# Kernel tuning notes

Measured on AMD Instinct MI355X. Metric: run time of the kernel, lower is better.

Reference implementation:

```python
import jax, jax.numpy as jnp
import numpy as np

N_HEAD = 16

def setup_inputs() -> dict:
    key = jax.random.key(0)
    ks = jax.random.split(key, 4)
    B, S, D = 2, 2048, 2048
    return {
        "hidden_states": jax.random.normal(ks[0], (B, S, D), dtype=jnp.float32),
        "attention_mask": jnp.ones((B, S), dtype=jnp.float32),
        "W_attn": jax.random.normal(ks[1], (D, 3 * D), dtype=jnp.float32) * (D ** -0.5),
        "b_attn": jnp.zeros((3 * D,), dtype=jnp.float32),
        "W_proj": jax.random.normal(ks[2], (D, D), dtype=jnp.float32) * (D ** -0.5),
        "b_proj": jnp.zeros((D,), dtype=jnp.float32),
        "lambda_param": jnp.float32(0.8),
    }

def reference(hidden_states, attention_mask, W_attn, b_attn, W_proj, b_proj, lambda_param):
    B, S, D = hidden_states.shape
    H = N_HEAD
    hd = D // H          # full head dim (used by V and for the scale)
    qd = hd // 2         # q/k per-head dim after the dual chunk
    scale = hd ** -0.5

    qkv = hidden_states @ W_attn + b_attn            # [B,S,3D]
    q, k, v = jnp.split(qkv, 3, axis=-1)
    q1, q2 = jnp.split(q, 2, axis=-1)                # each [B,S,D/2]
    k1, k2 = jnp.split(k, 2, axis=-1)

    def heads(x, d):  # [B,S,H*d] -> [B,H,S,d]
        return x.reshape(B, S, H, d).transpose(0, 2, 1, 3)

    q1, q2 = heads(q1, qd), heads(q2, qd)
    k1, k2 = heads(k1, qd), heads(k2, qd)
    v = heads(v, hd)

    # additive mask: (1 - m) * -10000, broadcast over heads and query dim
    mask = (1.0 - attention_mask)[:, None, None, :] * -10000.0  # [B,1,1,S]

    s1 = jnp.einsum("bhqd,bhkd->bhqk", q1, k1) * scale + mask
    s2 = jnp.einsum("bhqd,bhkd->bhqk", q2, k2) * scale + mask
    w = jax.nn.softmax(s1, axis=-1) - lambda_param * jax.nn.softmax(s2, axis=-1)

    out = jnp.einsum("bhqk,bhkd->bhqd", w, v)        # [B,H,S,hd]
    out = out.transpose(0, 2, 1, 3).reshape(B, S, D)
    return out @ W_proj + b_proj
```

## Files before the change

### kernel.cpp

```cpp
#include <hip/hip_runtime.h>
#include <hip/hip_bf16.h>

typedef __attribute__((ext_vector_type(8))) short bf16x8;
typedef __attribute__((ext_vector_type(8))) unsigned short u16x8;
typedef __attribute__((ext_vector_type(4))) float f32x4;

__device__ __forceinline__ unsigned short f2bf(float f) {
  union { float f; unsigned int i; } v; v.f = f;
  unsigned int r = v.i + 0x7FFFu + ((v.i >> 16) & 1u);
  return (unsigned short)(r >> 16);
}
__device__ __forceinline__ unsigned int pack2bf_rn(float a, float b) {
  union { float f; unsigned int i; } x, y; x.f = a; y.f = b;
  return ((x.i + 0x8000u) >> 16) | ((y.i + 0x8000u) & 0xFFFF0000u);
}
__device__ __forceinline__ unsigned int cvtpk(float a, float b) {
  unsigned int r;
  asm("v_cvt_pk_bf16_f32 %0, %1, %2" : "=v"(r) : "v"(a), "v"(b));
  return r;
}
__device__ __forceinline__ float fexp2(float x) {
  float r;
  asm("v_exp_f32 %0, %1" : "=v"(r) : "v"(x));
  return r;
}
__device__ __forceinline__ void gll16(const unsigned short* g, unsigned short* l) {
  __builtin_amdgcn_global_load_lds(
      (const __attribute__((address_space(1))) unsigned int*)g,
      (__attribute__((address_space(3))) unsigned int*)l, 16, 0, 0);
}

__global__ void cvt_bf16_k(const float* __restrict__ in, unsigned short* __restrict__ out,
                           long n) {
  long i = ((long)blockIdx.x * 256 + threadIdx.x) * 8;
  if (i + 8 > n) return;
  float4 a = *(const float4*)(in + i);
  float4 b = *(const float4*)(in + i + 4);
  u16x8 o;
  o[0] = f2bf(a.x); o[1] = f2bf(a.y); o[2] = f2bf(a.z); o[3] = f2bf(a.w);
  o[4] = f2bf(b.x); o[5] = f2bf(b.y); o[6] = f2bf(b.z); o[7] = f2bf(b.w);
  *(u16x8*)(out + i) = o;
}

__global__ void cvt_transpose_k(const float* __restrict__ in, unsigned short* __restrict__ out,
                                long in_rs, long out_rs) {
  __shared__ unsigned short tile[32][33];
  int c0 = blockIdx.x * 32, r0 = blockIdx.y * 32;
  int tx = threadIdx.x & 31, ty = threadIdx.x >> 5;
#pragma unroll
  for (int i = 0; i < 32; i += 8)
    tile[ty + i][tx] = f2bf(in[(long)(r0 + ty + i) * in_rs + c0 + tx]);
  __syncthreads();
#pragma unroll
  for (int i = 0; i < 32; i += 8)
    out[(long)(c0 + ty + i) * out_rs + r0 + tx] = tile[tx][ty + i];
}

__global__ __launch_bounds__(256) void gemm_qkv(
    const unsigned short* __restrict__ A,
    const unsigned short* __restrict__ Bt,
    const float* __restrict__ bias,
    unsigned short* __restrict__ qQ,
    unsigned short* __restrict__ k1p, unsigned short* __restrict__ k2p,
    unsigned short* __restrict__ vp) {
  const int K = 2048;
  __shared__ unsigned short As[128 * 32];
  __shared__ unsigned short Bs[128 * 32];
  const int m0 = blockIdx.y * 128, n0 = blockIdx.x * 128;
  const int tid = threadIdx.x, lane = tid & 63, wave = tid >> 6;
  const int wm = (wave >> 1) * 64, wn = (wave & 1) * 64;
  const int quad = lane >> 4, l15 = lane & 15;
  const int ar = tid >> 2, ak = (tid & 3) * 8;

  f32x4 acc[4][4] = {};
  const unsigned short* Ap = A + (long)(m0 + ar) * K + ak;
  const unsigned short* Bp = Bt + (long)(n0 + ar) * K + ak;
  unsigned short* AsW = As + wave * 512;
  unsigned short* BsW = Bs + wave * 512;

  for (int kb = 0; kb < K; kb += 32) {
    __syncthreads();
    gll16(Ap + kb, AsW);
    gll16(Ap + (long)64 * K + kb, AsW + 2048);
    gll16(Bp + kb, BsW);
    gll16(Bp + (long)64 * K + kb, BsW + 2048);
    __syncthreads();
    bf16x8 af[4], bfr[4];
#pragma unroll
    for (int t = 0; t < 4; t++)
      af[t] = *(const bf16x8*)&As[(wm + t * 16 + l15) * 32 + quad * 8];
#pragma unroll
    for (int t = 0; t < 4; t++)
      bfr[t] = *(const bf16x8*)&Bs[(wn + t * 16 + l15) * 32 + quad * 8];
#pragma unroll
    for (int i = 0; i < 4; i++)
#pragma unroll
      for (int j = 0; j < 4; j++)
        acc[i][j] = __builtin_amdgcn_mfma_f32_16x16x32_bf16(af[i], bfr[j], acc[i][j], 0, 0, 0);
  }

  const int ncol = n0 + wn;
  if (ncol < 2048) {
#pragma unroll
    for (int j = 0; j < 4; j++) {
      int n = ncol + j * 16 + l15;
      float bv = bias[n];
#pragma unroll
      for (int i = 0; i < 4; i++) {
        int mr = m0 + wm + i * 16 + quad * 4;
#pragma unroll
        for (int r = 0; r < 4; r++)
          qQ[(long)(mr + r) * 2048 + n] = f2bf(acc[i][j][r] + bv);
      }
    }
  } else if (ncol < 4096) {
    unsigned short* kp = (ncol >= 3072) ? k2p : k1p;
#pragma unroll
    for (int j = 0; j < 4; j++) {
      int n = ncol + j * 16 + l15;
      float bv = bias[n];
      int kk = (n - 2048) & 1023;
      int h = kk >> 6, c = (kk >> 3) & 7, e = kk & 7;
#pragma unroll
      for (int i = 0; i < 4; i++) {
        int mr = m0 + wm + i * 16 + quad * 4;
        int b = mr >> 11, s = mr & 2047;
        long tb2 = ((long)(b * 16 + h) * 32 + (s >> 6)) * 4096 + e;
        int row0 = s & 63;
#pragma unroll
        for (int r = 0; r < 4; r++) {
          int row = row0 + r;
          kp[tb2 + row * 64 + ((c ^ (row & 7)) << 3)] = f2bf(acc[i][j][r] + bv);
        }
      }
    }
  } else {
#pragma unroll
    for (int j = 0; j < 4; j++) {
      int n = ncol + j * 16 + l15;
      float bv = bias[n];
      int vv = n - 4096;
      int h = vv >> 7, d = vv & 127;
#pragma unroll
      for (int i = 0; i < 4; i++) {
        int mr = m0 + wm + i * 16 + quad * 4;
        int b = mr >> 11, s = mr & 2047;
        int cc = (s & 63) >> 3;
        long dst = ((long)(b * 16 + h) * 32 + (s >> 6)) * 8192 + d * 64 +
                   ((cc ^ (d & 7)) << 3) + (quad & 1) * 4;
        uint2 st;
        st.x = pack2bf_rn(acc[i][j][0] + bv, acc[i][j][1] + bv);
        st.y = pack2bf_rn(acc[i][j][2] + bv, acc[i][j][3] + bv);
        *(uint2*)&vp[dst] = st;
      }
    }
  }
}

__global__ __launch_bounds__(256) void gemm_bt_f32(
    const unsigned short* __restrict__ A,
    const unsigned short* __restrict__ Bt,
    const float* __restrict__ bias,
    float* __restrict__ C, int K, int ldc) {
  __shared__ unsigned short As[128 * 32];
  __shared__ unsigned short Bs[128 * 32];
  const int m0 = blockIdx.y * 128, n0 = blockIdx.x * 128;
  const int tid = threadIdx.x, lane = tid & 63, wave = tid >> 6;
  const int wm = (wave >> 1) * 64, wn = (wave & 1) * 64;
  const int quad = lane >> 4, l15 = lane & 15;
  const int ar = tid >> 2, ak = (tid & 3) * 8;

  f32x4 acc[4][4] = {};
  const unsigned short* Ap = A + (long)(m0 + ar) * K + ak;
  const unsigned short* Bp = Bt + (long)(n0 + ar) * K + ak;
  unsigned short* AsW = As + wave * 512;
  unsigned short* BsW = Bs + wave * 512;

  for (int kb = 0; kb < K; kb += 32) {
    __syncthreads();
    gll16(Ap + kb, AsW);
    gll16(Ap + (long)64 * K + kb, AsW + 2048);
    gll16(Bp + kb, BsW);
    gll16(Bp + (long)64 * K + kb, BsW + 2048);
    __syncthreads();
    bf16x8 af[4], bfr[4];
#pragma unroll
    for (int t = 0; t < 4; t++)
      af[t] = *(const bf16x8*)&As[(wm + t * 16 + l15) * 32 + quad * 8];
#pragma unroll
    for (int t = 0; t < 4; t++)
      bfr[t] = *(const bf16x8*)&Bs[(wn + t * 16 + l15) * 32 + quad * 8];
#pragma unroll
    for (int i = 0; i < 4; i++)
#pragma unroll
      for (int j = 0; j < 4; j++)
        acc[i][j] = __builtin_amdgcn_mfma_f32_16x16x32_bf16(af[i], bfr[j], acc[i][j], 0, 0, 0);
  }
#pragma unroll
  for (int j = 0; j < 4; j++) {
    int n = n0 + wn + j * 16 + l15;
    float bv = bias[n];
#pragma unroll
    for (int i = 0; i < 4; i++) {
      int mr = m0 + wm + i * 16 + quad * 4;
#pragma unroll
      for (int r = 0; r < 4; r++)
        C[(long)(mr + r) * ldc + n] = acc[i][j][r] + bv;
    }
  }
}

__global__ __launch_bounds__(256, 2) void attn_k(
    const unsigned short* __restrict__ qQ,
    const unsigned short* __restrict__ k1p,
    const unsigned short* __restrict__ k2p,
    const unsigned short* __restrict__ vp,
    const float* __restrict__ mask,
    const float* __restrict__ lamp,
    unsigned short* __restrict__ out) {
  __shared__ unsigned short k1s[2 * 4096];
  __shared__ unsigned short k2s[2 * 4096];
  __shared__ unsigned short vts[2 * 8192];
  __shared__ unsigned short pls[4 * 2048];
  const int bid = blockIdx.x;
  const int wgid = (bid & 7) * 64 + (bid >> 3);
  const int bh = wgid >> 4;
  const int q0 = (wgid & 15) * 128;
  const int b = bh >> 4, h = bh & 15;
  const int tid = threadIdx.x, lane = tid & 63, wave = tid >> 6;
  const int quad = lane >> 4, l15 = lane & 15;
  const long rowq = (long)b * 2048 + q0;
  const int sw = l15 & 7;

  bf16x8 aq1[2][2], aq2[2][2];
#pragma unroll
  for (int qt = 0; qt < 2; qt++) {
    const unsigned short* qr =
        qQ + (rowq + wave * 32 + qt * 16 + l15) * 2048 + h * 64 + quad * 8;
    aq1[qt][0] = *(const bf16x8*)qr;
    aq1[qt][1] = *(const bf16x8*)(qr + 32);
    aq2[qt][0] = *(const bf16x8*)(qr + 1024);
    aq2[qt][1] = *(const bf16x8*)(qr + 1056);
  }
  f32x4 o1[2][8] = {}, o2[2][8] = {};
  f32x4 l1a[2] = {}, l2a[2] = {};
  bf16x8 ones;
#pragma unroll
  for (int e = 0; e < 8; e++) ones[e] = (short)0x3F80;
  const float SL = 0.08838834764831845f * 1.4426950408889634f;
  const float ML = 1.4426950408889634e4f;
  const long tb = (long)bh * 32;
  unsigned short* pw = pls + wave * 2048;

  {
    const unsigned short* k1t = k1p + tb * 4096 + tid * 8;
    const unsigned short* k2t = k2p + tb * 4096 + tid * 8;
    const unsigned short* vtt = vp + tb * 8192 + tid * 8;
    gll16(k1t, k1s + wave * 512);
    gll16(k1t + 2048, k1s + 2048 + wave * 512);
    gll16(k2t, k2s + wave * 512);
    gll16(k2t + 2048, k2s + 2048 + wave * 512);
#pragma unroll
    for (int rr = 0; rr < 4; rr++)
      gll16(vtt + rr * 2048, vts + rr * 2048 + wave * 512);
  }

  for (int t = 0; t < 32; t++) {
    const int cb = t & 1;
    __syncthreads();
    float4 mq[4];
#pragma unroll
    for (int nt = 0; nt < 4; nt++)
      mq[nt] = *(const float4*)(mask + (long)b * 2048 + t * 64 + nt * 16 + quad * 4);
    if (t < 31) {
      const unsigned short* k1t = k1p + (tb + t + 1) * 4096 + tid * 8;
      const unsigned short* k2t = k2p + (tb + t + 1) * 4096 + tid * 8;
      const unsigned short* vtt = vp + (tb + t + 1) * 8192 + tid * 8;
      unsigned short* d1 = k1s + (cb ^ 1) * 4096 + wave * 512;
      unsigned short* d2 = k2s + (cb ^ 1) * 4096 + wave * 512;
      unsigned short* dv = vts + (cb ^ 1) * 8192 + wave * 512;
      gll16(k1t, d1);
      gll16(k1t + 2048, d1 + 2048);
      gll16(k2t, d2);
      gll16(k2t + 2048, d2 + 2048);
#pragma unroll
      for (int rr = 0; rr < 4; rr++)
        gll16(vtt + rr * 2048, dv + rr * 2048);
    }

#pragma unroll
    for (int half = 0; half < 2; half++) {
      f32x4 s1[2][2] = {}, s2[2][2] = {};
#pragma unroll
      for (int np = 0; np < 2; np++) {
        const int row = cb * 4096 + (half * 32 + np * 16 + l15) * 64;
#pragma unroll
        for (int ks = 0; ks < 2; ks++) {
          const int p = ((ks * 4 + quad) ^ sw) * 8;
          bf16x8 kf1 = *(const bf16x8*)&k1s[row + p];
          bf16x8 kf2 = *(const bf16x8*)&k2s[row + p];
#pragma unroll
          for (int qt = 0; qt < 2; qt++) {
            s1[qt][np] = __builtin_amdgcn_mfma_f32_16x16x32_bf16(kf1, aq1[qt][ks], s1[qt][np], 0, 0, 0);
            s2[qt][np] = __builtin_amdgcn_mfma_f32_16x16x32_bf16(kf2, aq2[qt][ks], s2[qt][np], 0, 0, 0);
          }
        }
      }
      float ma[2][4];
#pragma unroll
      for (int np = 0; np < 2; np++)
#pragma unroll
        for (int r = 0; r < 4; r++)
          ma[np][r] = fmaf(((const float*)&mq[half * 2 + np])[r], ML, -ML);
#pragma unroll
      for (int qt = 0; qt < 2; qt++)
#pragma unroll
        for (int np = 0; np < 2; np++) {
          const int addr = l15 * 32 + (((np * 4 + quad) ^ sw) << 2);
          uint2 w1, w2;
          w1.x = cvtpk(fexp2(fmaf(s1[qt][np][0], SL, ma[np][0])),
                       fexp2(fmaf(s1[qt][np][1], SL, ma[np][1])));
          w1.y = cvtpk(fexp2(fmaf(s1[qt][np][2], SL, ma[np][2])),
                       fexp2(fmaf(s1[qt][np][3], SL, ma[np][3])));
          w2.x = cvtpk(fexp2(fmaf(s2[qt][np][0], SL, ma[np][0])),
                       fexp2(fmaf(s2[qt][np][1], SL, ma[np][1])));
          w2.y = cvtpk(fexp2(fmaf(s2[qt][np][2], SL, ma[np][2])),
                       fexp2(fmaf(s2[qt][np][3], SL, ma[np][3])));
          *(uint2*)&pw[(qt * 2 + 0) * 512 + addr] = w1;
          *(uint2*)&pw[(qt * 2 + 1) * 512 + addr] = w2;
        }
      asm volatile("s_waitcnt lgkmcnt(0)" ::: "memory");
      bf16x8 f1[2], f2[2];
      {
        const int ra = l15 * 32 + (((quad * 2 + 0) ^ sw) << 2);
        const int rb = l15 * 32 + (((quad * 2 + 1) ^ sw) << 2);
#pragma unroll
        for (int qt = 0; qt < 2; qt++) {
          union { bf16x8 v; uint2 u2[2]; } g1, g2;
          g1.u2[0] = *(const uint2*)&pw[(qt * 2 + 0) * 512 + ra];
          g1.u2[1] = *(const uint2*)&pw[(qt * 2 + 0) * 512 + rb];
          g2.u2[0] = *(const uint2*)&pw[(qt * 2 + 1) * 512 + ra];
          g2.u2[1] = *(const uint2*)&pw[(qt * 2 + 1) * 512 + rb];
          f1[qt] = g1.v; f2[qt] = g2.v;
        }
      }
#pragma unroll
      for (int qt = 0; qt < 2; qt++) {
        l1a[qt] = __builtin_amdgcn_mfma_f32_16x16x32_bf16(ones, f1[qt], l1a[qt], 0, 0, 0);
        l2a[qt] = __builtin_amdgcn_mfma_f32_16x16x32_bf16(ones, f2[qt], l2a[qt], 0, 0, 0);
      }
#pragma unroll
      for (int dn = 0; dn < 8; dn++) {
        const int pp = ((half * 4 + quad) ^ sw) * 8;
        bf16x8 vf = *(const bf16x8*)&vts[cb * 8192 + (dn * 16 + l15) * 64 + pp];
#pragma unroll
        for (int qt = 0; qt < 2; qt++) {
          o1[qt][dn] = __builtin_amdgcn_mfma_f32_16x16x32_bf16(vf, f1[qt], o1[qt][dn], 0, 0, 0);
          o2[qt][dn] = __builtin_amdgcn_mfma_f32_16x16x32_bf16(vf, f2[qt], o2[qt][dn], 0, 0, 0);
        }
      }
      asm volatile("s_waitcnt lgkmcnt(0)" ::: "memory");
    }
  }
  float lam = lamp[0];
#pragma unroll
  for (int qt = 0; qt < 2; qt++) {
    float i1 = 1.f / l1a[qt][0], i2 = lam / l2a[qt][0];
    unsigned short* orow =
        out + (rowq + wave * 32 + qt * 16 + l15) * 2048 + h * 128 + quad * 4;
#pragma unroll
    for (int dn = 0; dn < 8; dn++) {
      uint2 st;
      st.x = cvtpk(o1[qt][dn][0] * i1 - o2[qt][dn][0] * i2,
                   o1[qt][dn][1] * i1 - o2[qt][dn][1] * i2);
      st.y = cvtpk(o1[qt][dn][2] * i1 - o2[qt][dn][2] * i2,
                   o1[qt][dn][3] * i1 - o2[qt][dn][3] * i2);
      *(uint2*)(orow + dn * 16) = st;
    }
  }
}

extern "C" void kernel_launch(void* const* d_in, const int* in_sizes, int n_in,
                              void* d_out, int out_size, void* d_ws, size_t ws_size,
                              hipStream_t stream) {
  (void)in_sizes; (void)n_in; (void)out_size; (void)ws_size;
  const float* hs   = (const float*)d_in[0];
  const float* mask = (const float*)d_in[1];
  const float* Wa   = (const float*)d_in[2];
  const float* ba   = (const float*)d_in[3];
  const float* Wp   = (const float*)d_in[4];
  const float* bp   = (const float*)d_in[5];
  const float* lam  = (const float*)d_in[6];
  float* out = (float*)d_out;
  unsigned short* ws = (unsigned short*)d_ws;

  unsigned short* hsb = ws;
  unsigned short* WtA = hsb + (long)4096 * 2048;
  unsigned short* WtP = WtA + (long)6144 * 2048;
  unsigned short* qQ  = WtP + (long)2048 * 2048;
  unsigned short* K1p = qQ + (long)4096 * 2048;
  unsigned short* K2p = K1p + (long)2 * 16 * 2048 * 64;
  unsigned short* Vp  = K2p + (long)2 * 16 * 2048 * 64;
  unsigned short* att = hsb;

  cvt_bf16_k<<<4096, 256, 0, stream>>>(hs, hsb, (long)4096 * 2048);
  cvt_transpose_k<<<dim3(192, 64), 256, 0, stream>>>(Wa, WtA, 6144, 2048);
  cvt_transpose_k<<<dim3(64, 64), 256, 0, stream>>>(Wp, WtP, 2048, 2048);
  gemm_qkv<<<dim3(48, 32), 256, 0, stream>>>(hsb, WtA, ba, qQ, K1p, K2p, Vp);
  attn_k<<<512, 256, 0, stream>>>(qQ, K1p, K2p, Vp, mask, lam, att);
  gemm_bt_f32<<<dim3(16, 32), 256, 0, stream>>>(att, WtP, bp, out, 2048, 2048);
}
```

Baseline: 459.7 us.

## Merge prep kernels, remap GEMM tiles across XCDs, drop attention waitcnts

Folds the three conversion and transpose launches into one prep kernel, which removes launch gaps between them. Both GEMMs now index tiles through a 1D grid with an XCD-aware remap (blockIdx & 7), so neighbouring tiles share L2 on the same chiplet. Two explicit lgkmcnt waits in the attention inner loop are removed, leaving LDS ordering to the compiler. That last change risks a read-after-write hazard on the shared P buffer if the compiler does not insert the needed wait.

```diff
diff --git a/kernel.cpp b/kernel.cpp
--- a/kernel.cpp
+++ b/kernel.cpp
@@ -30,22 +30,9 @@
       (__attribute__((address_space(3))) unsigned int*)l, 16, 0, 0);
 }
 
-__global__ void cvt_bf16_k(const float* __restrict__ in, unsigned short* __restrict__ out,
-                           long n) {
-  long i = ((long)blockIdx.x * 256 + threadIdx.x) * 8;
-  if (i + 8 > n) return;
-  float4 a = *(const float4*)(in + i);
-  float4 b = *(const float4*)(in + i + 4);
-  u16x8 o;
-  o[0] = f2bf(a.x); o[1] = f2bf(a.y); o[2] = f2bf(a.z); o[3] = f2bf(a.w);
-  o[4] = f2bf(b.x); o[5] = f2bf(b.y); o[6] = f2bf(b.z); o[7] = f2bf(b.w);
-  *(u16x8*)(out + i) = o;
-}
-
-__global__ void cvt_transpose_k(const float* __restrict__ in, unsigned short* __restrict__ out,
-                                long in_rs, long out_rs) {
-  __shared__ unsigned short tile[32][33];
-  int c0 = blockIdx.x * 32, r0 = blockIdx.y * 32;
+__device__ __forceinline__ void transpose32(const float* in, unsigned short* out,
+                                            long in_rs, long out_rs, int c0, int r0,
+                                            unsigned short (*tile)[33]) {
   int tx = threadIdx.x & 31, ty = threadIdx.x >> 5;
 #pragma unroll
   for (int i = 0; i < 32; i += 8)
@@ -54,6 +41,30 @@
 #pragma unroll
   for (int i = 0; i < 32; i += 8)
     out[(long)(c0 + ty + i) * out_rs + r0 + tx] = tile[tx][ty + i];
+}
+
+__global__ void prep_k(const float* __restrict__ hs, unsigned short* __restrict__ hsb,
+                       const float* __restrict__ Wa, unsigned short* __restrict__ WtA,
+                       const float* __restrict__ Wp, unsigned short* __restrict__ WtP) {
+  __shared__ unsigned short tile[32][33];
+  const int bid = blockIdx.x;
+  if (bid < 4096) {
+    long i = ((long)bid * 256 + threadIdx.x) * 8;
+    float4 a = *(const float4*)(hs + i);
+    float4 b = *(const float4*)(hs + i + 4);
+    u16x8 o;
+    o[0] = f2bf(a.x); o[1] = f2bf(a.y); o[2] = f2bf(a.z); o[3] = f2bf(a.w);
+    o[4] = f2bf(b.x); o[5] = f2bf(b.y); o[6] = f2bf(b.z); o[7] = f2bf(b.w);
+    *(u16x8*)(hsb + i) = o;
+  } else if (bid < 16384) {
+    int r = bid - 4096;
+    int bx = r % 192, by = r / 192;
+    transpose32(Wa, WtA, 6144, 2048, bx * 32, by * 32, tile);
+  } else {
+    int r = bid - 16384;
+    int bx = r & 63, by = r >> 6;
+    transpose32(Wp, WtP, 2048, 2048, bx * 32, by * 32, tile);
+  }
 }
 
 __global__ __launch_bounds__(256) void gemm_qkv(
@@ -66,7 +77,8 @@
   const int K = 2048;
   __shared__ unsigned short As[128 * 32];
   __shared__ unsigned short Bs[128 * 32];
-  const int m0 = blockIdx.y * 128, n0 = blockIdx.x * 128;
+  const int wgid = (blockIdx.x & 7) * 192 + (blockIdx.x >> 3);
+  const int m0 = (wgid / 48) * 128, n0 = (wgid % 48) * 128;
   const int tid = threadIdx.x, lane = tid & 63, wave = tid >> 6;
   const int wm = (wave >> 1) * 64, wn = (wave & 1) * 64;
   const int quad = lane >> 4, l15 = lane & 15;
@@ -164,7 +176,8 @@
     float* __restrict__ C, int K, int ldc) {
   __shared__ unsigned short As[128 * 32];
   __shared__ unsigned short Bs[128 * 32];
-  const int m0 = blockIdx.y * 128, n0 = blockIdx.x * 128;
+  const int wgid = (blockIdx.x & 7) * 64 + (blockIdx.x >> 3);
+  const int m0 = (wgid >> 4) * 128, n0 = (wgid & 15) * 128;
   const int tid = threadIdx.x, lane = tid & 63, wave = tid >> 6;
   const int wm = (wave >> 1) * 64, wn = (wave & 1) * 64;
   const int quad = lane >> 4, l15 = lane & 15;
@@ -329,7 +342,6 @@
           *(uint2*)&pw[(qt * 2 + 0) * 512 + addr] = w1;
           *(uint2*)&pw[(qt * 2 + 1) * 512 + addr] = w2;
         }
-      asm volatile("s_waitcnt lgkmcnt(0)" ::: "memory");
       bf16x8 f1[2], f2[2];
       {
         const int ra = l15 * 32 + (((quad * 2 + 0) ^ sw) << 2);
@@ -359,7 +371,6 @@
           o2[qt][dn] = __builtin_amdgcn_mfma_f32_16x16x32_bf16(vf, f2[qt], o2[qt][dn], 0, 0, 0);
         }
       }
-      asm volatile("s_waitcnt lgkmcnt(0)" ::: "memory");
     }
   }
   float lam = lamp[0];
@@ -403,10 +414,8 @@
   unsigned short* Vp  = K2p + (long)2 * 16 * 2048 * 64;
   unsigned short* att = hsb;
 
-  cvt_bf16_k<<<4096, 256, 0, stream>>>(hs, hsb, (long)4096 * 2048);
-  cvt_transpose_k<<<dim3(192, 64), 256, 0, stream>>>(Wa, WtA, 6144, 2048);
-  cvt_transpose_k<<<dim3(64, 64), 256, 0, stream>>>(Wp, WtP, 2048, 2048);
-  gemm_qkv<<<dim3(48, 32), 256, 0, stream>>>(hsb, WtA, ba, qQ, K1p, K2p, Vp);
+  prep_k<<<20480, 256, 0, stream>>>(hs, hsb, Wa, WtA, Wp, WtP);
+  gemm_qkv<<<1536, 256, 0, stream>>>(hsb, WtA, ba, qQ, K1p, K2p, Vp);
   attn_k<<<512, 256, 0, stream>>>(qQ, K1p, K2p, Vp, mask, lam, att);
-  gemm_bt_f32<<<dim3(16, 32), 256, 0, stream>>>(att, WtP, bp, out, 2048, 2048);
-}
+  gemm_bt_f32<<<512, 256, 0, stream>>>(att, WtP, bp, out, 2048, 2048);
+}
```

Result: faster. 449.1 us (-2.3%).
